# Kernel optimization log

Measured on AMD Instinct MI355X. Metric: run time of the kernel, lower is better.

Reference implementation:

```python
import jax, jax.numpy as jnp
import numpy as np

B, S, H, K = 8, 2048, 768, 128
FILTERS = (1, 3, 5)
C = H // len(FILTERS)  # 256 channels per conv, concat -> H
LN_EPS = 1e-05
COS_EPS = 1e-08


def setup_inputs() -> dict:
    key = jax.random.key(0)
    ks = jax.random.split(key, 16)
    mk = lambda k, shape: jax.random.normal(k, shape, dtype=jnp.float32) * 0.02
    return {
        "representation": jax.random.normal(ks[0], (B, S, H), dtype=jnp.float32),
        "src_mask": jnp.ones((B, S), dtype=jnp.float32),
        # conv weights stored as [k, H_in, C_out] for lax 1D conv (torch Conv2d(1,C,(k,H)))
        "enc_conv_w1": mk(ks[1], (1, H, C)),
        "enc_conv_w3": mk(ks[2], (3, H, C)),
        "enc_conv_w5": mk(ks[3], (5, H, C)),
        "ln_g": jnp.ones((H,), jnp.float32),
        "ln_b": jnp.zeros((H,), jnp.float32),
        "enc_lin_w": mk(ks[4], (H, H)),   # torch Linear weight [out,in]
        "enc_tr_w": mk(ks[5], (K, H)),
        "dec_tr_w": mk(ks[6], (H, K)),
        "dec_conv_w1": mk(ks[7], (1, H, C)),
        "dec_conv_w3": mk(ks[8], (3, H, C)),
        "dec_conv_w5": mk(ks[9], (5, H, C)),
        "dec_lin_w": mk(ks[10], (H, H)),
        "out_lin_w": mk(ks[11], (H, H)),
    }


def _multi_conv(x, ws):
    # x: [B, S, H]; each w: [k, H, C]; torch pads (k//2, 0) -> same-length for odd k
    outs = []
    for w in ws:
        k = w.shape[0]
        outs.append(jax.lax.conv_general_dilated(
            x, w, window_strides=(1,), padding=[(k // 2, k // 2)],
            dimension_numbers=("NWC", "WIO", "NWC")))
    return jnp.concatenate(outs, axis=-1)  # [B, S, H]


def _layernorm(x, g, b):
    mu = jnp.mean(x, axis=-1, keepdims=True)
    var = jnp.mean((x - mu) ** 2, axis=-1, keepdims=True)
    return (x - mu) * jax.lax.rsqrt(var + LN_EPS) * g + b


def reference(representation, src_mask, enc_conv_w1, enc_conv_w3, enc_conv_w5,
              ln_g, ln_b, enc_lin_w, enc_tr_w, dec_tr_w,
              dec_conv_w1, dec_conv_w3, dec_conv_w5, dec_lin_w, out_lin_w):
    # ---- AutoEncoder (dropout layers are identity in eval mode) ----
    h = _multi_conv(representation, (enc_conv_w1, enc_conv_w3, enc_conv_w5))
    h = _layernorm(h + representation, ln_g, ln_b)
    h = jnp.tanh(h @ enc_lin_w.T)
    location = h @ enc_tr_w.T            # [B, S, K] (encode_out)
    d = location @ dec_tr_w.T            # [B, S, H]
    d = _multi_conv(d, (dec_conv_w1, dec_conv_w3, dec_conv_w5))
    d = jnp.tanh(d @ dec_lin_w.T)
    decode_out = d @ out_lin_w.T         # [B, S, H]

    # ---- banded pairwise cosine similarity (fuses the torch shift loop) ----
    # torch loop writes dis_matrix[b, i, i+s+1] = cos(loc[b, i+s+1], loc[b, i])
    # for s in range(max_act_len), i.e. the strict upper band of the symmetric
    # pairwise cosine-similarity matrix with offsets 1..max_act_len.
    normed = location / jnp.maximum(
        jnp.sqrt(jnp.sum(location * location, axis=-1, keepdims=True)), COS_EPS)
    sim = jnp.einsum("bid,bjd->bij", normed, normed)  # [B, S, S]
    offs = jnp.arange(S)[None, :] - jnp.arange(S)[:, None]  # j - i
    max_act_len = jnp.max(jnp.sum(src_mask, axis=-1)).astype(jnp.int32)
    band = (offs >= 1) & (offs <= max_act_len)        # [S, S]
    dis_matrix = jnp.where(band[None], sim, 0.0)
    src_dis_mask = src_mask[:, :, None] * src_mask[:, None, :]
    act_dis_tags = band[None].astype(jnp.float32) * src_dis_mask
    return (location, dis_matrix, act_dis_tags, decode_out)
```

## Files before the change

### kernel.cpp

```cpp
#include <hip/hip_runtime.h>

#define B_   8
#define S_   2048
#define H_   768
#define K_   128
#define C_   256
#define SH_  2052
#define MTOK (B_*S_)

typedef __attribute__((ext_vector_type(8))) short short8;
typedef __attribute__((ext_vector_type(4))) float f32x4;

typedef __attribute__((address_space(1))) const void gvoid;
typedef __attribute__((address_space(3))) void lvoid;

__device__ __forceinline__ void gload16(const void* g, void* l) {
    __builtin_amdgcn_global_load_lds((gvoid*)g, (lvoid*)l, 16, 0, 0);
}

__device__ __forceinline__ ushort f2b(float f) {
    union { float f; unsigned u; } v; v.f = f;
    unsigned r = v.u + 0x7fffu + ((v.u >> 16) & 1u);
    return (ushort)(r >> 16);
}
__device__ __forceinline__ float b2f(ushort u) {
    union { unsigned u; float f; } v; v.u = ((unsigned)u) << 16;
    return v.f;
}
__device__ __forceinline__ float fast_tanh(float x) {
    float e = __expf(2.f * x);
    return 1.f - 2.f / (e + 1.f);
}


struct CvtE { const float* src; ushort* dst; int n; int kh; int sld; };

struct PrepP {
    const float* mask; int* Lp; ushort* lh;
    const float* rep;  ushort* xh;
    CvtE e[12];
};

__global__ __launch_bounds__(256) void k_prep(PrepP p) {
    const int tid = threadIdx.x;
    const int y = blockIdx.y;
    if (y == 0) {
        if (blockIdx.x == 0) {
            __shared__ float sh[4];
            float mx = 0.f;
            for (int b = 0; b < B_; ++b) {
                float s = 0.f;
                for (int q = tid; q < 512; q += 256) {
                    const float4 v = ((const float4*)(p.mask + b * S_))[q];
                    s += v.x + v.y + v.z + v.w;
                }
#pragma unroll
                for (int off = 32; off; off >>= 1) s += __shfl_xor(s, off);
                if ((tid & 63) == 0) sh[tid >> 6] = s;
                __syncthreads();
                if (tid == 0) mx = fmaxf(mx, sh[0] + sh[1] + sh[2] + sh[3]);
                __syncthreads();
            }
            if (tid == 0) *p.Lp = (int)mx;
            for (int i = tid; i < B_ * 4 * K_; i += 256) {
                const int b = i >> 9;
                const int rc = i & 511;
                const int rr = rc >> 7;
                const int cc = rc & 127;
                const int row = (rr < 2) ? rr : (2048 + rr);
                p.lh[((size_t)b * SH_ + row) * K_ + cc] = 0;
            }
        } else {
            int i = (blockIdx.x - 1) * 256 + tid;
            const int stride = (gridDim.x - 1) * 256;
            const int n4 = B_ * SH_ * H_ / 4;
            for (; i < n4; i += stride) {
                const int idx = i * 4;
                const int h = idx % H_;
                const int rs = idx / H_;
                const int s = rs % SH_;
                const int b = rs / SH_;
                ushort4 o; o.x = 0; o.y = 0; o.z = 0; o.w = 0;
                if (s >= 2 && s < S_ + 2) {
                    const float4 v = *(const float4*)(p.rep + ((size_t)b * S_ + (s - 2)) * H_ + h);
                    o.x = f2b(v.x); o.y = f2b(v.y); o.z = f2b(v.z); o.w = f2b(v.w);
                }
                *(ushort4*)(p.xh + idx) = o;
            }
        }
    } else {
        const CvtE e = p.e[y - 1];
        int i = blockIdx.x * 256 + tid;
        const int stride = gridDim.x * 256;
        for (; i < e.n; i += stride) {
            if (e.kh < 0) {
                e.dst[i] = 0;
            } else if (e.kh) {
                const int c = i / e.kh;
                const int r = i - c * e.kh;
                e.dst[i] = f2b(e.src[r * e.sld + c]);
            } else {
                e.dst[i] = f2b(e.src[i]);
            }
        }
    }
}


struct CompE { const ushort* w; int wld; int woff; ushort* o; int old_; int koff; };
struct CompP { const ushort* dtrT; CompE e[9]; };

__global__ __launch_bounds__(256) void k_compw(CompP p) {
    __shared__ __align__(16) ushort As[128 * 64];
    __shared__ __align__(16) ushort Bs[128 * 64];
    const CompE e = p.e[blockIdx.y];
    const int tid = threadIdx.x;
    const int w = tid >> 6, lane = tid & 63;
    const int l15 = lane & 15, lk = lane >> 4;
    const int wr = w >> 1, wc = w & 1;
    const int n_base = blockIdx.x * 128;
    f32x4 acc[4][4] = {};
    const int srow = lane >> 3;
    const int scol = (lane & 7) * 8;

    for (int kt = 0; kt < 12; ++kt) {
        const int kk = kt << 6;
#pragma unroll
        for (int q = 0; q < 4; ++q) {
            const int r = w * 32 + q * 8;
            gload16(p.dtrT + (size_t)(r + srow) * 768 + kk + scol, As + r * 64);
            gload16(e.w + (size_t)(n_base + r + srow) * e.wld + e.woff + kk + scol, Bs + r * 64);
        }
        __syncthreads();
#pragma unroll
        for (int ks = 0; ks < 2; ++ks) {
            short8 af[4], bfr[4];
#pragma unroll
            for (int i = 0; i < 4; ++i)
                af[i] = *(const short8*)(As + (wr * 64 + i * 16 + l15) * 64 + ks * 32 + 8 * lk);
#pragma unroll
            for (int j = 0; j < 4; ++j)
                bfr[j] = *(const short8*)(Bs + (wc * 64 + j * 16 + l15) * 64 + ks * 32 + 8 * lk);
#pragma unroll
            for (int i = 0; i < 4; ++i)
#pragma unroll
                for (int j = 0; j < 4; ++j)
                    acc[i][j] = __builtin_amdgcn_mfma_f32_16x16x32_bf16(af[i], bfr[j], acc[i][j], 0, 0, 0);
        }
        __syncthreads();
    }
#pragma unroll
    for (int i = 0; i < 4; ++i)
#pragma unroll
        for (int j = 0; j < 4; ++j)
#pragma unroll
            for (int jj = 0; jj < 4; ++jj) {
                const int jr = wr * 64 + i * 16 + 4 * lk + jj;
                const int c  = n_base + wc * 64 + j * 16 + l15;
                e.o[(size_t)c * e.old_ + e.koff + jr] = f2b(acc[i][j][jj]);
            }
}


struct G3P {
    const ushort* A;
    const ushort* W0;
    const ushort* W1;
    const ushort* W2;
    int lda;
    ushort* outB; int ldoB;
    int nMtiles;
};

__global__ __launch_bounds__(512, 2) void g3(G3P p) {
    constexpr int TPT = 12;
    constexpr int LDA = 768;
    constexpr int ASEG = 1024;
    constexpr int BSEG = 2048;
    constexpr int BUFE = (ASEG + BSEG) * 8;
    __shared__ __align__(16) ushort lds[3][BUFE];

    const int tid = threadIdx.x;
    const int w = tid >> 6, lane = tid & 63;
    const int l15 = lane & 15, lk = lane >> 4;
    const int wr = w >> 2, wc = w & 3;
    const int axor = l15 & 7;

    const int nM = p.nMtiles;
    int idx = blockIdx.x;
    int br;
    if (idx < nM) br = 2;
    else if (idx < 2 * nM) { br = 1; idx -= nM; }
    else { br = 0; idx -= 2 * nM; }
    idx = (idx & 7) * 16 + (idx >> 3);
    const int m_base = idx * 128;
    const int n_base = br * 256;
    const int nt = TPT * (2 * br + 1);
    const int Ktot = LDA * (2 * br + 1);
    const ushort* Wt = (br == 0) ? p.W0 : (br == 1) ? p.W1 : p.W2;
    const int arow0 = m_base + ((m_base >> 11) << 2) + (2 - br);

    auto stage1 = [&](int kt, int bufi, int q) {
        const int tap = kt / TPT;
        const int h0 = (kt - tap * TPT) << 6;
        if (q < 2) {
            const int seg = q * 512 + tid;
            const int row = seg >> 3;
            const int slot = (seg & 7) ^ (row & 7);
            gload16(p.A + (size_t)(arow0 + tap + row) * LDA + h0 + slot * 8,
                    &lds[bufi][seg * 8]);
        } else {
            const int seg = (q - 2) * 512 + tid;
            const int row = seg >> 3;
            const int slot = (seg & 7) ^ (row & 7);
            gload16(Wt + (size_t)row * Ktot + (kt << 6) + slot * 8,
                    &lds[bufi][ASEG * 8 + seg * 8]);
        }
    };
    auto stage = [&](int kt, int bufi) {
#pragma unroll
        for (int q = 0; q < 6; ++q) stage1(kt, bufi, q);
    };

    f32x4 acc[4][4] = {};

    stage(0, 0);
    stage(1, 1);

    int buf = 0;
    for (int t = 0; t < nt; ++t) {
        const ushort* Ab = &lds[buf][0];
        const ushort* Bb = &lds[buf][ASEG * 8];
        if (t + 1 < nt) asm volatile("s_waitcnt vmcnt(6)" ::: "memory");
        else            asm volatile("s_waitcnt vmcnt(0)" ::: "memory");
        __builtin_amdgcn_sched_barrier(0);
        asm volatile("s_barrier" ::: "memory");
        __builtin_amdgcn_sched_barrier(0);

        int nbuf = buf + 2; if (nbuf >= 3) nbuf -= 3;
        const bool sb = (t + 2 < nt);

#pragma unroll
        for (int ks = 0; ks < 2; ++ks) {
            short8 bq[4], aq[4];
#pragma unroll
            for (int ni = 0; ni < 4; ++ni)
                bq[ni] = *(const short8*)(Bb + (wc * 64 + ni * 16 + l15) * 64 + ((((ks << 2) | lk) ^ axor) << 3));
#pragma unroll
            for (int mi = 0; mi < 4; ++mi)
                aq[mi] = *(const short8*)(Ab + (wr * 64 + mi * 16 + l15) * 64 + ((((ks << 2) | lk) ^ axor) << 3));
            if (sb) { stage1(t + 2, nbuf, 3 * ks); stage1(t + 2, nbuf, 3 * ks + 1); stage1(t + 2, nbuf, 3 * ks + 2); }
            asm volatile("s_waitcnt lgkmcnt(0)" ::: "memory");
            __builtin_amdgcn_sched_barrier(0);
            __builtin_amdgcn_s_setprio(1);
#pragma unroll
            for (int mi = 0; mi < 4; ++mi)
#pragma unroll
                for (int ni = 0; ni < 4; ++ni)
                    acc[mi][ni] = __builtin_amdgcn_mfma_f32_16x16x32_bf16(aq[mi], bq[ni], acc[mi][ni], 0, 0, 0);
            __builtin_amdgcn_s_setprio(0);
            __builtin_amdgcn_sched_barrier(0);
        }
        ++buf; if (buf == 3) buf = 0;
    }

#pragma unroll
    for (int mi = 0; mi < 4; ++mi)
#pragma unroll
        for (int ni = 0; ni < 4; ++ni)
#pragma unroll
            for (int jj = 0; jj < 4; ++jj) {
                const int r = m_base + wr * 64 + mi * 16 + 4 * lk + jj;
                const int n = n_base + wc * 64 + ni * 16 + l15;
                p.outB[(size_t)r * p.ldoB + n] = f2b(acc[mi][ni][jj]);
            }
}


struct G4P {
    const ushort* A;
    const ushort* W;
    int Ktot;
    int lda;
    ushort* outB; int ldoB;
    float*  outF; int ldoF;
    int act;
    int haloA;
};

__global__ __launch_bounds__(256, 2) void g4(G4P p) {
    constexpr int ASEG = 1024;
    constexpr int BSEG = 1536;
    __shared__ __align__(16) ushort lds[2][(ASEG + BSEG) * 8];

    const int tid = threadIdx.x;
    const int w = tid >> 6, lane = tid & 63;
    const int l15 = lane & 15, lk = lane >> 4;
    const int wr = w >> 1, wc = w & 1;
    const int axor = l15 & 7;
    const int bx = (blockIdx.x & 7) * 16 + (blockIdx.x >> 3);
    const int m_base = bx * 128;
    const int n_base = blockIdx.y * 192;
    const int nt = p.Ktot >> 6;
    const int abase = p.haloA ? (m_base + ((m_base >> 11) << 2)) : m_base;

    auto stage = [&](int kt, int bufi) {
        const int kk = kt << 6;
        ushort* Ab = &lds[bufi][0];
        ushort* Bb = &lds[bufi][ASEG * 8];
#pragma unroll
        for (int q = 0; q < 4; ++q) {
            const int seg = q * 256 + tid;
            const int row = seg >> 3;
            const int s = (seg & 7) ^ (row & 7);
            gload16(p.A + (size_t)(abase + row) * p.lda + kk + s * 8, Ab + seg * 8);
        }
#pragma unroll
        for (int q = 0; q < 6; ++q) {
            const int seg = q * 256 + tid;
            const int row = seg >> 3;
            const int s = (seg & 7) ^ (row & 7);
            gload16(p.W + (size_t)(n_base + row) * p.Ktot + kk + s * 8, Bb + seg * 8);
        }
    };

    f32x4 acc[4][6] = {};

    stage(0, 0);
    stage(1, 1);

    for (int t = 0; t < nt; ++t) {
        const int cur = t & 1;
        const ushort* Ab = &lds[cur][0];
        const ushort* Bb = &lds[cur][ASEG * 8];
        if (t + 1 < nt) asm volatile("s_waitcnt vmcnt(10)" ::: "memory");
        else            asm volatile("s_waitcnt vmcnt(0)" ::: "memory");
        __builtin_amdgcn_sched_barrier(0);
        asm volatile("s_barrier" ::: "memory");
        __builtin_amdgcn_sched_barrier(0);

        short8 af[4][2], bf[6][2];
#pragma unroll
        for (int mi = 0; mi < 4; ++mi)
#pragma unroll
            for (int ks = 0; ks < 2; ++ks)
                af[mi][ks] = *(const short8*)(Ab + (wr * 64 + mi * 16 + l15) * 64 + ((((ks << 2) | lk) ^ axor) << 3));
#pragma unroll
        for (int ni = 0; ni < 6; ++ni)
#pragma unroll
            for (int ks = 0; ks < 2; ++ks)
                bf[ni][ks] = *(const short8*)(Bb + (wc * 96 + ni * 16 + l15) * 64 + ((((ks << 2) | lk) ^ axor) << 3));
        asm volatile("s_waitcnt lgkmcnt(0)" ::: "memory");
        __builtin_amdgcn_sched_barrier(0);
        asm volatile("s_barrier" ::: "memory");
        __builtin_amdgcn_sched_barrier(0);
        if (t + 2 < nt) stage(t + 2, cur);
        __builtin_amdgcn_sched_barrier(0);
        __builtin_amdgcn_s_setprio(1);
#pragma unroll
        for (int mi = 0; mi < 4; ++mi)
#pragma unroll
            for (int ni = 0; ni < 6; ++ni) {
                acc[mi][ni] = __builtin_amdgcn_mfma_f32_16x16x32_bf16(af[mi][0], bf[ni][0], acc[mi][ni], 0, 0, 0);
                acc[mi][ni] = __builtin_amdgcn_mfma_f32_16x16x32_bf16(af[mi][1], bf[ni][1], acc[mi][ni], 0, 0, 0);
            }
        __builtin_amdgcn_s_setprio(0);
        __builtin_amdgcn_sched_barrier(0);
    }

#pragma unroll
    for (int mi = 0; mi < 4; ++mi)
#pragma unroll
        for (int ni = 0; ni < 6; ++ni)
#pragma unroll
            for (int jj = 0; jj < 4; ++jj) {
                const int r = m_base + wr * 64 + mi * 16 + 4 * lk + jj;
                const int n = n_base + wc * 96 + ni * 16 + l15;
                float v = acc[mi][ni][jj];
                if (p.act) v = fast_tanh(v);
                if (p.outF) p.outF[(size_t)r * p.ldoF + n] = v;
                if (p.outB) p.outB[(size_t)r * p.ldoB + n] = f2b(v);
            }
}


struct GLP {
    const ushort* A;
    const ushort* Wt;
    float* outF;
    ushort* outH;
    ushort* outN;
};

__global__ __launch_bounds__(256) void gemm_loc(GLP p) {
    __shared__ __align__(16) ushort As[64 * 64];
    __shared__ __align__(16) ushort Bs[128 * 64];
    __shared__ float rowss[64][2];
    const int tid = threadIdx.x;
    const int w = tid >> 6, lane = tid & 63;
    const int l15 = lane & 15, lk = lane >> 4;
    const int bx = (blockIdx.x & 7) * 32 + (blockIdx.x >> 3);
    const int m_base = bx * 64;
    const int wr = w >> 1, wc = w & 1;
    f32x4 acc[2][4] = {};
    const int srow = lane >> 3;
    const int scol = (lane & 7) * 8;

    for (int kt = 0; kt < 12; ++kt) {
        const int kk = kt << 6;
#pragma unroll
        for (int q = 0; q < 2; ++q) {
            const int r = w * 16 + q * 8;
            gload16(p.A + (size_t)(m_base + r + srow) * H_ + kk + scol, As + r * 64);
        }
#pragma unroll
        for (int q = 0; q < 4; ++q) {
            const int r = w * 32 + q * 8;
            gload16(p.Wt + (size_t)(r + srow) * H_ + kk + scol, Bs + r * 64);
        }
        __syncthreads();
#pragma unroll
        for (int ks = 0; ks < 2; ++ks) {
            short8 af[2], bfr[4];
#pragma unroll
            for (int i = 0; i < 2; ++i)
                af[i] = *(const short8*)(As + (wr * 32 + i * 16 + l15) * 64 + ks * 32 + 8 * lk);
#pragma unroll
            for (int j = 0; j < 4; ++j)
                bfr[j] = *(const short8*)(Bs + (wc * 64 + j * 16 + l15) * 64 + ks * 32 + 8 * lk);
#pragma unroll
            for (int i = 0; i < 2; ++i)
#pragma unroll
                for (int j = 0; j < 4; ++j)
                    acc[i][j] = __builtin_amdgcn_mfma_f32_16x16x32_bf16(af[i], bfr[j], acc[i][j], 0, 0, 0);
        }
        __syncthreads();
    }

#pragma unroll
    for (int i = 0; i < 2; ++i)
#pragma unroll
        for (int jj = 0; jj < 4; ++jj) {
            float s = acc[i][0][jj] * acc[i][0][jj] + acc[i][1][jj] * acc[i][1][jj]
                    + acc[i][2][jj] * acc[i][2][jj] + acc[i][3][jj] * acc[i][3][jj];
#pragma unroll
            for (int off = 1; off < 16; off <<= 1) s += __shfl_xor(s, off);
            if (l15 == 0) rowss[wr * 32 + i * 16 + 4 * lk + jj][wc] = s;
        }
    __syncthreads();

    const int bb4 = ((m_base >> 11) << 2) + 2;
#pragma unroll
    for (int i = 0; i < 2; ++i)
#pragma unroll
        for (int j = 0; j < 4; ++j)
#pragma unroll
            for (int jj = 0; jj < 4; ++jj) {
                const int lr = wr * 32 + i * 16 + 4 * lk + jj;
                const int r  = m_base + lr;
                const int n  = wc * 64 + j * 16 + l15;
                const float v = acc[i][j][jj];
                const float ss = rowss[lr][0] + rowss[lr][1];
                const float sc = 1.f / fmaxf(sqrtf(ss), 1e-8f);
                p.outF[(size_t)r * K_ + n] = v;
                p.outH[(size_t)(r + bb4) * K_ + n] = f2b(v);
                p.outN[(size_t)r * K_ + n] = f2b(v * sc);
            }
}


__global__ __launch_bounds__(192) void k_ln(const ushort* __restrict__ conv,
                                            const float* __restrict__ rep,
                                            const float* __restrict__ gw,
                                            const float* __restrict__ bw,
                                            ushort* __restrict__ out) {
    const int row = blockIdx.x;
    const int tid = threadIdx.x;
    const int h = tid * 4;
    const ushort4 cv = *(const ushort4*)(conv + (size_t)row * H_ + h);
    const float4  rv = *(const float4*)(rep + (size_t)row * H_ + h);
    float v[4] = { b2f(cv.x) + rv.x, b2f(cv.y) + rv.y, b2f(cv.z) + rv.z, b2f(cv.w) + rv.w };
    float s1 = v[0] + v[1] + v[2] + v[3];
    float s2 = v[0]*v[0] + v[1]*v[1] + v[2]*v[2] + v[3]*v[3];
#pragma unroll
    for (int off = 32; off; off >>= 1) { s1 += __shfl_xor(s1, off); s2 += __shfl_xor(s2, off); }
    __shared__ float sh[6];
    const int wid = tid >> 6, lane = tid & 63;
    if (lane == 0) { sh[wid] = s1; sh[3 + wid] = s2; }
    __syncthreads();
    s1 = sh[0] + sh[1] + sh[2];
    s2 = sh[3] + sh[4] + sh[5];
    const float mu  = s1 * (1.f / H_);
    const float var = s2 * (1.f / H_) - mu * mu;
    const float rs  = rsqrtf(var + 1e-5f);
    const float4 gv = *(const float4*)(gw + h);
    const float4 bv = *(const float4*)(bw + h);
    ushort4 o;
    o.x = f2b((v[0] - mu) * rs * gv.x + bv.x);
    o.y = f2b((v[1] - mu) * rs * gv.y + bv.y);
    o.z = f2b((v[2] - mu) * rs * gv.z + bv.z);
    o.w = f2b((v[3] - mu) * rs * gv.w + bv.w);
    *(ushort4*)(out + (size_t)row * H_ + h) = o;
}


__global__ __launch_bounds__(256) void k_simtags(const ushort* __restrict__ normed,
                                                 const float* __restrict__ mask,
                                                 const int* __restrict__ Lp,
                                                 float* __restrict__ dis,
                                                 float* __restrict__ tags) {
    const int wid = threadIdx.x >> 6, lane = threadIdx.x & 63;
    const int l15 = lane & 15, lk = lane >> 4;
    const int b   = blockIdx.z;
    const int i0b = blockIdx.x * 64;
    const int i0  = i0b + wid * 16;
    const int j0  = blockIdx.y * 64;
    const int L   = *Lp;
    f32x4 acc[4] = {};
    if ((j0 + 63 >= i0b + 1) && (j0 <= i0b + 63 + L)) {
        const ushort* nb = normed + (size_t)b * S_ * K_;
#pragma unroll
        for (int kt = 0; kt < 4; ++kt) {
            const int kk = kt * 32;
            const short8 a = *(const short8*)(nb + (size_t)(i0 + l15) * K_ + kk + 8 * lk);
#pragma unroll
            for (int j = 0; j < 4; ++j) {
                const short8 bfr = *(const short8*)(nb + (size_t)(j0 + j * 16 + l15) * K_ + kk + 8 * lk);
                acc[j] = __builtin_amdgcn_mfma_f32_16x16x32_bf16(a, bfr, acc[j], 0, 0, 0);
            }
        }
    }
    const float* mb = mask + b * S_;
    float* dp = dis  + (size_t)b * S_ * S_;
    float* tp = tags + (size_t)b * S_ * S_;
#pragma unroll
    for (int j = 0; j < 4; ++j) {
#pragma unroll
        for (int jj = 0; jj < 4; ++jj) {
            const int i  = i0 + 4 * lk + jj;
            const int jc = j0 + j * 16 + l15;
            const int d  = jc - i;
            const bool band = (d >= 1 && d <= L);
            dp[(size_t)i * S_ + jc] = band ? acc[j][jj] : 0.f;
            tp[(size_t)i * S_ + jc] = band ? mb[i] * mb[jc] : 0.f;
        }
    }
}


extern "C" void kernel_launch(void* const* d_in, const int* in_sizes, int n_in,
                              void* d_out, int out_size, void* d_ws, size_t ws_size,
                              hipStream_t stream) {
    const float* rep  = (const float*)d_in[0];
    const float* mask = (const float*)d_in[1];
    const float* ew1  = (const float*)d_in[2];
    const float* ew3  = (const float*)d_in[3];
    const float* ew5  = (const float*)d_in[4];
    const float* lng  = (const float*)d_in[5];
    const float* lnb  = (const float*)d_in[6];
    const float* elin = (const float*)d_in[7];
    const float* etr  = (const float*)d_in[8];
    const float* dtr  = (const float*)d_in[9];
    const float* dw1  = (const float*)d_in[10];
    const float* dw3  = (const float*)d_in[11];
    const float* dw5  = (const float*)d_in[12];
    const float* dlin = (const float*)d_in[13];
    const float* olin = (const float*)d_in[14];

    float* out_loc = (float*)d_out;
    float* out_dis = out_loc + (size_t)B_ * S_ * K_;
    float* out_tag = out_dis + (size_t)B_ * S_ * S_;
    float* out_dec = out_tag + (size_t)B_ * S_ * S_;

    char* ws = (char*)d_ws;
    size_t off = 0;
    auto alloc = [&](size_t bytes) -> char* {
        char* p = ws + off;
        off += (bytes + 255) & ~(size_t)255;
        return p;
    };
    int*    Lp    = (int*)alloc(256);
    ushort* Xh    = (ushort*)alloc((size_t)B_ * SH_ * H_ * 2);
    ushort* bufLh = (ushort*)alloc((size_t)B_ * SH_ * K_ * 2);
    ushort* wte1  = (ushort*)alloc((size_t)C_ * 768 * 2);
    ushort* wte3  = (ushort*)alloc((size_t)C_ * 2304 * 2);
    ushort* wte5  = (ushort*)alloc((size_t)C_ * 3840 * 2);
    ushort* wtd1  = (ushort*)alloc((size_t)C_ * 768 * 2);
    ushort* wtd3  = (ushort*)alloc((size_t)C_ * 2304 * 2);
    ushort* wtd5  = (ushort*)alloc((size_t)C_ * 3840 * 2);
    ushort* welin = (ushort*)alloc((size_t)H_ * H_ * 2);
    ushort* wetr  = (ushort*)alloc((size_t)K_ * H_ * 2);
    ushort* dtrT  = (ushort*)alloc((size_t)K_ * H_ * 2);
    ushort* wdlin = (ushort*)alloc((size_t)H_ * H_ * 2);
    ushort* wolin = (ushort*)alloc((size_t)H_ * H_ * 2);
    ushort* Wc    = (ushort*)alloc((size_t)H_ * 640 * 2);
    ushort* bufB  = (ushort*)alloc((size_t)MTOK * H_ * 2);
    ushort* bufC  = (ushort*)alloc((size_t)MTOK * H_ * 2);
    ushort* bufD  = (ushort*)alloc((size_t)MTOK * H_ * 2);
    ushort* bufN  = (ushort*)alloc((size_t)MTOK * K_ * 2);
    if (ws_size < off) return;

    PrepP pp;
    pp.mask = mask; pp.Lp = Lp; pp.lh = bufLh;
    pp.rep = rep; pp.xh = Xh;
    pp.e[0]  = { ew1,  wte1, 768 * C_,  768,  C_ };
    pp.e[1]  = { ew3,  wte3, 2304 * C_, 2304, C_ };
    pp.e[2]  = { ew5,  wte5, 3840 * C_, 3840, C_ };
    pp.e[3]  = { dw1,  wtd1, 768 * C_,  768,  C_ };
    pp.e[4]  = { dw3,  wtd3, 2304 * C_, 2304, C_ };
    pp.e[5]  = { dw5,  wtd5, 3840 * C_, 3840, C_ };
    pp.e[6]  = { elin, welin, H_ * H_, 0, 0 };
    pp.e[7]  = { etr,  wetr,  K_ * H_, 0, 0 };
    pp.e[8]  = { dlin, wdlin, H_ * H_, 0, 0 };
    pp.e[9]  = { olin, wolin, H_ * H_, 0, 0 };
    pp.e[10] = { dtr,  dtrT,  K_ * H_, 768, K_ };
    pp.e[11] = { nullptr, Wc, H_ * 640, -1, 0 };
    k_prep<<<dim3(2048, 13), 256, 0, stream>>>(pp);

    {
        CompP cp; cp.dtrT = dtrT;
        cp.e[0] = { wtd1, 768,  0, Wc + (size_t)0 * 640,   640, 2 * 128 };
        for (int t = 0; t < 3; ++t)
            cp.e[1 + t] = { wtd3, 2304, t * 768, Wc + (size_t)256 * 640, 640, (1 + t) * 128 };
        for (int t = 0; t < 5; ++t)
            cp.e[4 + t] = { wtd5, 3840, t * 768, Wc + (size_t)512 * 640, 640, t * 128 };
        k_compw<<<dim3(2, 9), 256, 0, stream>>>(cp);
    }

    {
        G3P p{}; p.A = Xh; p.W0 = wte1; p.W1 = wte3; p.W2 = wte5;
        p.lda = H_; p.outB = bufB; p.ldoB = H_; p.nMtiles = MTOK / 128;
        g3<<<3 * (MTOK / 128), 512, 0, stream>>>(p);
    }
    k_ln<<<MTOK, 192, 0, stream>>>(bufB, rep, lng, lnb, bufC);
    {
        G4P p{}; p.A = bufC; p.W = welin; p.Ktot = H_; p.lda = H_;
        p.outB = bufD; p.ldoB = H_; p.act = 1;
        g4<<<dim3(MTOK / 128, H_ / 192), 256, 0, stream>>>(p);
    }
    {
        GLP p{ bufD, wetr, out_loc, bufLh, bufN };
        gemm_loc<<<MTOK / 64, 256, 0, stream>>>(p);
    }
    {
        G4P p{}; p.A = bufLh; p.W = Wc; p.Ktot = 640; p.lda = K_;
        p.outB = bufB; p.ldoB = H_; p.haloA = 1;
        g4<<<dim3(MTOK / 128, H_ / 192), 256, 0, stream>>>(p);
    }
    {
        G4P p{}; p.A = bufB; p.W = wdlin; p.Ktot = H_; p.lda = H_;
        p.outB = bufC; p.ldoB = H_; p.act = 1;
        g4<<<dim3(MTOK / 128, H_ / 192), 256, 0, stream>>>(p);
    }
    {
        G4P p{}; p.A = bufC; p.W = wolin; p.Ktot = H_; p.lda = H_;
        p.outF = out_dec; p.ldoF = H_;
        g4<<<dim3(MTOK / 128, H_ / 192), 256, 0, stream>>>(p);
    }
    k_simtags<<<dim3(S_ / 64, S_ / 64, B_), 256, 0, stream>>>(bufN, mask, Lp, out_dis, out_tag);
}
```

Before: 374.9 us.

## Shrink encoder conv GEMM tile to 64x256 with 256 threads and double buffering

Replaces the 512-thread 128x256-tile encoder conv kernel with a 256-thread 64x256-tile version that uses two LDS buffers instead of three. Each iteration now loads all fragments up front, synchronises, then issues the next stage's loads into the freed buffer before running the MFMAs. The change also drops the XCD-style block index swizzle in g4 and gemm_loc. Smaller tiles double the grid and may help occupancy and load balance across the three conv branches, but they lower weight reuse per tile and add an extra barrier per k-step.

```diff
diff --git a/kernel.cpp b/kernel.cpp
--- a/kernel.cpp
+++ b/kernel.cpp
@@ -169,57 +169,51 @@
     const ushort* W2;
     int lda;
     ushort* outB; int ldoB;
-    int nMtiles;
 };
 
-__global__ __launch_bounds__(512, 2) void g3(G3P p) {
+__global__ __launch_bounds__(256, 2) void g3b(G3P p) {
     constexpr int TPT = 12;
     constexpr int LDA = 768;
-    constexpr int ASEG = 1024;
+    constexpr int ASEG = 512;
     constexpr int BSEG = 2048;
-    constexpr int BUFE = (ASEG + BSEG) * 8;
-    __shared__ __align__(16) ushort lds[3][BUFE];
+    __shared__ __align__(16) ushort lds[2][(ASEG + BSEG) * 8];
 
     const int tid = threadIdx.x;
-    const int w = tid >> 6, lane = tid & 63;
+    const int wc = tid >> 6, lane = tid & 63;
     const int l15 = lane & 15, lk = lane >> 4;
-    const int wr = w >> 2, wc = w & 3;
     const int axor = l15 & 7;
 
-    const int nM = p.nMtiles;
     int idx = blockIdx.x;
     int br;
-    if (idx < nM) br = 2;
-    else if (idx < 2 * nM) { br = 1; idx -= nM; }
-    else { br = 0; idx -= 2 * nM; }
-    idx = (idx & 7) * 16 + (idx >> 3);
-    const int m_base = idx * 128;
+    if (idx < 256) br = 2;
+    else if (idx < 512) { br = 1; idx -= 256; }
+    else { br = 0; idx -= 512; }
+    const int m_base = idx * 64;
     const int n_base = br * 256;
     const int nt = TPT * (2 * br + 1);
     const int Ktot = LDA * (2 * br + 1);
     const ushort* Wt = (br == 0) ? p.W0 : (br == 1) ? p.W1 : p.W2;
     const int arow0 = m_base + ((m_base >> 11) << 2) + (2 - br);
 
-    auto stage1 = [&](int kt, int bufi, int q) {
+    auto stage = [&](int kt, int bufi) {
         const int tap = kt / TPT;
         const int h0 = (kt - tap * TPT) << 6;
-        if (q < 2) {
-            const int seg = q * 512 + tid;
+        ushort* Ab = &lds[bufi][0];
+        ushort* Bb = &lds[bufi][ASEG * 8];
+#pragma unroll
+        for (int q = 0; q < 2; ++q) {
+            const int seg = q * 256 + tid;
             const int row = seg >> 3;
-            const int slot = (seg & 7) ^ (row & 7);
-            gload16(p.A + (size_t)(arow0 + tap + row) * LDA + h0 + slot * 8,
-                    &lds[bufi][seg * 8]);
-        } else {
-            const int seg = (q - 2) * 512 + tid;
+            const int s = (seg & 7) ^ (row & 7);
+            gload16(p.A + (size_t)(arow0 + tap + row) * LDA + h0 + s * 8, Ab + seg * 8);
+        }
+#pragma unroll
+        for (int q = 0; q < 8; ++q) {
+            const int seg = q * 256 + tid;
             const int row = seg >> 3;
-            const int slot = (seg & 7) ^ (row & 7);
-            gload16(Wt + (size_t)row * Ktot + (kt << 6) + slot * 8,
-                    &lds[bufi][ASEG * 8 + seg * 8]);
-        }
-    };
-    auto stage = [&](int kt, int bufi) {
-#pragma unroll
-        for (int q = 0; q < 6; ++q) stage1(kt, bufi, q);
+            const int s = (seg & 7) ^ (row & 7);
+            gload16(Wt + (size_t)row * Ktot + (kt << 6) + s * 8, Bb + seg * 8);
+        }
     };
 
     f32x4 acc[4][4] = {};
@@ -227,41 +221,43 @@
     stage(0, 0);
     stage(1, 1);
 
-    int buf = 0;
     for (int t = 0; t < nt; ++t) {
-        const ushort* Ab = &lds[buf][0];
-        const ushort* Bb = &lds[buf][ASEG * 8];
-        if (t + 1 < nt) asm volatile("s_waitcnt vmcnt(6)" ::: "memory");
+        const int cur = t & 1;
+        const ushort* Ab = &lds[cur][0];
+        const ushort* Bb = &lds[cur][ASEG * 8];
+        if (t + 1 < nt) asm volatile("s_waitcnt vmcnt(10)" ::: "memory");
         else            asm volatile("s_waitcnt vmcnt(0)" ::: "memory");
         __builtin_amdgcn_sched_barrier(0);
         asm volatile("s_barrier" ::: "memory");
         __builtin_amdgcn_sched_barrier(0);
 
-        int nbuf = buf + 2; if (nbuf >= 3) nbuf -= 3;
-        const bool sb = (t + 2 < nt);
-
-#pragma unroll
-        for (int ks = 0; ks < 2; ++ks) {
-            short8 bq[4], aq[4];
-#pragma unroll
-            for (int ni = 0; ni < 4; ++ni)
-                bq[ni] = *(const short8*)(Bb + (wc * 64 + ni * 16 + l15) * 64 + ((((ks << 2) | lk) ^ axor) << 3));
-#pragma unroll
-            for (int mi = 0; mi < 4; ++mi)
-                aq[mi] = *(const short8*)(Ab + (wr * 64 + mi * 16 + l15) * 64 + ((((ks << 2) | lk) ^ axor) << 3));
-            if (sb) { stage1(t + 2, nbuf, 3 * ks); stage1(t + 2, nbuf, 3 * ks + 1); stage1(t + 2, nbuf, 3 * ks + 2); }
-            asm volatile("s_waitcnt lgkmcnt(0)" ::: "memory");
-            __builtin_amdgcn_sched_barrier(0);
-            __builtin_amdgcn_s_setprio(1);
-#pragma unroll
-            for (int mi = 0; mi < 4; ++mi)
-#pragma unroll
-                for (int ni = 0; ni < 4; ++ni)
-                    acc[mi][ni] = __builtin_amdgcn_mfma_f32_16x16x32_bf16(aq[mi], bq[ni], acc[mi][ni], 0, 0, 0);
-            __builtin_amdgcn_s_setprio(0);
-            __builtin_amdgcn_sched_barrier(0);
-        }
-        ++buf; if (buf == 3) buf = 0;
+        short8 af[4][2], bf[4][2];
+#pragma unroll
+        for (int mi = 0; mi < 4; ++mi)
+#pragma unroll
+            for (int ks = 0; ks < 2; ++ks)
+                af[mi][ks] = *(const short8*)(Ab + (mi * 16 + l15) * 64 + ((((ks << 2) | lk) ^ axor) << 3));
+#pragma unroll
+        for (int ni = 0; ni < 4; ++ni)
+#pragma unroll
+            for (int ks = 0; ks < 2; ++ks)
+                bf[ni][ks] = *(const short8*)(Bb + (wc * 64 + ni * 16 + l15) * 64 + ((((ks << 2) | lk) ^ axor) << 3));
+        asm volatile("s_waitcnt lgkmcnt(0)" ::: "memory");
+        __builtin_amdgcn_sched_barrier(0);
+        asm volatile("s_barrier" ::: "memory");
+        __builtin_amdgcn_sched_barrier(0);
+        if (t + 2 < nt) stage(t + 2, cur);
+        __builtin_amdgcn_sched_barrier(0);
+        __builtin_amdgcn_s_setprio(1);
+#pragma unroll
+        for (int mi = 0; mi < 4; ++mi)
+#pragma unroll
+            for (int ni = 0; ni < 4; ++ni) {
+                acc[mi][ni] = __builtin_amdgcn_mfma_f32_16x16x32_bf16(af[mi][0], bf[ni][0], acc[mi][ni], 0, 0, 0);
+                acc[mi][ni] = __builtin_amdgcn_mfma_f32_16x16x32_bf16(af[mi][1], bf[ni][1], acc[mi][ni], 0, 0, 0);
+            }
+        __builtin_amdgcn_s_setprio(0);
+        __builtin_amdgcn_sched_barrier(0);
     }
 
 #pragma unroll
@@ -270,7 +266,7 @@
         for (int ni = 0; ni < 4; ++ni)
 #pragma unroll
             for (int jj = 0; jj < 4; ++jj) {
-                const int r = m_base + wr * 64 + mi * 16 + 4 * lk + jj;
+                const int r = m_base + mi * 16 + 4 * lk + jj;
                 const int n = n_base + wc * 64 + ni * 16 + l15;
                 p.outB[(size_t)r * p.ldoB + n] = f2b(acc[mi][ni][jj]);
             }
@@ -298,8 +294,7 @@
     const int l15 = lane & 15, lk = lane >> 4;
     const int wr = w >> 1, wc = w & 1;
     const int axor = l15 & 7;
-    const int bx = (blockIdx.x & 7) * 16 + (blockIdx.x >> 3);
-    const int m_base = bx * 128;
+    const int m_base = blockIdx.x * 128;
     const int n_base = blockIdx.y * 192;
     const int nt = p.Ktot >> 6;
     const int abase = p.haloA ? (m_base + ((m_base >> 11) << 2)) : m_base;
@@ -399,8 +394,7 @@
     const int tid = threadIdx.x;
     const int w = tid >> 6, lane = tid & 63;
     const int l15 = lane & 15, lk = lane >> 4;
-    const int bx = (blockIdx.x & 7) * 32 + (blockIdx.x >> 3);
-    const int m_base = bx * 64;
+    const int m_base = blockIdx.x * 64;
     const int wr = w >> 1, wc = w & 1;
     f32x4 acc[2][4] = {};
     const int srow = lane >> 3;
@@ -629,8 +623,8 @@
 
     {
         G3P p{}; p.A = Xh; p.W0 = wte1; p.W1 = wte3; p.W2 = wte5;
-        p.lda = H_; p.outB = bufB; p.ldoB = H_; p.nMtiles = MTOK / 128;
-        g3<<<3 * (MTOK / 128), 512, 0, stream>>>(p);
+        p.lda = H_; p.outB = bufB; p.ldoB = H_;
+        g3b<<<768, 256, 0, stream>>>(p);
     }
     k_ln<<<MTOK, 192, 0, stream>>>(bufB, rep, lng, lnb, bufC);
     {
```

After: 383.6 us. 1.02x slower.

## Fold decoder linear weight into composed conv weight, removing one GEMM

Applied to the files above, without the earlier changes.

Precomputes Wz = dec_lin_w × (composed decoder transform+conv weight) with a new small GEMM kernel. The decoder conv GEMM and the following dec_lin GEMM become one K=640 GEMM with tanh applied directly. This removes a full 16K×768×768 GEMM and one intermediate buffer round-trip. It also drops the block-index swizzles in g3, g4 and gemm_loc, which changes L2 locality, and adds an extra bf16 rounding of the combined weight.

```diff
diff --git a/kernel.cpp b/kernel.cpp
--- a/kernel.cpp
+++ b/kernel.cpp
@@ -157,7 +157,61 @@
             for (int jj = 0; jj < 4; ++jj) {
                 const int jr = wr * 64 + i * 16 + 4 * lk + jj;
                 const int c  = n_base + wc * 64 + j * 16 + l15;
-                e.o[(size_t)c * e.old_ + e.koff + jr] = f2b(acc[i][j][jj]);
+                e.o[(size_t)(e.koff + jr) * e.old_ + c] = f2b(acc[i][j][jj]);
+            }
+}
+
+
+__global__ __launch_bounds__(256) void k_wz(const ushort* __restrict__ wdlin,
+                                            const ushort* __restrict__ WcT,
+                                            ushort* __restrict__ Wz) {
+    __shared__ __align__(16) ushort As[128 * 64];
+    __shared__ __align__(16) ushort Bs[128 * 64];
+    const int tid = threadIdx.x;
+    const int w = tid >> 6, lane = tid & 63;
+    const int l15 = lane & 15, lk = lane >> 4;
+    const int wr = w >> 1, wc = w & 1;
+    const int m_base = blockIdx.x * 128;
+    const int n_base = blockIdx.y * 128;
+    f32x4 acc[4][4] = {};
+    const int srow = lane >> 3;
+    const int scol = (lane & 7) * 8;
+
+    for (int kt = 0; kt < 12; ++kt) {
+        const int kk = kt << 6;
+#pragma unroll
+        for (int q = 0; q < 4; ++q) {
+            const int r = w * 32 + q * 8;
+            gload16(wdlin + (size_t)(m_base + r + srow) * 768 + kk + scol, As + r * 64);
+            gload16(WcT + (size_t)(n_base + r + srow) * 768 + kk + scol, Bs + r * 64);
+        }
+        __syncthreads();
+#pragma unroll
+        for (int ks = 0; ks < 2; ++ks) {
+            short8 af[4], bfr[4];
+#pragma unroll
+            for (int i = 0; i < 4; ++i)
+                af[i] = *(const short8*)(As + (wr * 64 + i * 16 + l15) * 64 + ks * 32 + 8 * lk);
+#pragma unroll
+            for (int j = 0; j < 4; ++j)
+                bfr[j] = *(const short8*)(Bs + (wc * 64 + j * 16 + l15) * 64 + ks * 32 + 8 * lk);
+#pragma unroll
+            for (int i = 0; i < 4; ++i)
+#pragma unroll
+                for (int j = 0; j < 4; ++j)
+                    acc[i][j] = __builtin_amdgcn_mfma_f32_16x16x32_bf16(af[i], bfr[j], acc[i][j], 0, 0, 0);
+        }
+        __syncthreads();
+    }
+#pragma unroll
+    for (int i = 0; i < 4; ++i)
+#pragma unroll
+        for (int j = 0; j < 4; ++j)
+#pragma unroll
+            for (int jj = 0; jj < 4; ++jj) {
+                const int o = m_base + wr * 64 + i * 16 + 4 * lk + jj;
+                const int k = n_base + wc * 64 + j * 16 + l15;
+                Wz[(size_t)o * 640 + k] = f2b(acc[i][j][jj]);
             }
 }
 
@@ -192,7 +246,6 @@
     if (idx < nM) br = 2;
     else if (idx < 2 * nM) { br = 1; idx -= nM; }
     else { br = 0; idx -= 2 * nM; }
-    idx = (idx & 7) * 16 + (idx >> 3);
     const int m_base = idx * 128;
     const int n_base = br * 256;
     const int nt = TPT * (2 * br + 1);
@@ -298,8 +351,7 @@
     const int l15 = lane & 15, lk = lane >> 4;
     const int wr = w >> 1, wc = w & 1;
     const int axor = l15 & 7;
-    const int bx = (blockIdx.x & 7) * 16 + (blockIdx.x >> 3);
-    const int m_base = bx * 128;
+    const int m_base = blockIdx.x * 128;
     const int n_base = blockIdx.y * 192;
     const int nt = p.Ktot >> 6;
     const int abase = p.haloA ? (m_base + ((m_base >> 11) << 2)) : m_base;
@@ -399,8 +451,7 @@
     const int tid = threadIdx.x;
     const int w = tid >> 6, lane = tid & 63;
     const int l15 = lane & 15, lk = lane >> 4;
-    const int bx = (blockIdx.x & 7) * 32 + (blockIdx.x >> 3);
-    const int m_base = bx * 64;
+    const int m_base = blockIdx.x * 64;
     const int wr = w >> 1, wc = w & 1;
     f32x4 acc[2][4] = {};
     const int srow = lane >> 3;
@@ -593,7 +644,8 @@
     ushort* dtrT  = (ushort*)alloc((size_t)K_ * H_ * 2);
     ushort* wdlin = (ushort*)alloc((size_t)H_ * H_ * 2);
     ushort* wolin = (ushort*)alloc((size_t)H_ * H_ * 2);
-    ushort* Wc    = (ushort*)alloc((size_t)H_ * 640 * 2);
+    ushort* WcT   = (ushort*)alloc((size_t)640 * H_ * 2);
+    ushort* Wz    = (ushort*)alloc((size_t)H_ * 640 * 2);
     ushort* bufB  = (ushort*)alloc((size_t)MTOK * H_ * 2);
     ushort* bufC  = (ushort*)alloc((size_t)MTOK * H_ * 2);
     ushort* bufD  = (ushort*)alloc((size_t)MTOK * H_ * 2);
@@ -614,18 +666,19 @@
     pp.e[8]  = { dlin, wdlin, H_ * H_, 0, 0 };
     pp.e[9]  = { olin, wolin, H_ * H_, 0, 0 };
     pp.e[10] = { dtr,  dtrT,  K_ * H_, 768, K_ };
-    pp.e[11] = { nullptr, Wc, H_ * 640, -1, 0 };
+    pp.e[11] = { nullptr, WcT, 640 * H_, -1, 0 };
     k_prep<<<dim3(2048, 13), 256, 0, stream>>>(pp);
 
     {
         CompP cp; cp.dtrT = dtrT;
-        cp.e[0] = { wtd1, 768,  0, Wc + (size_t)0 * 640,   640, 2 * 128 };
+        cp.e[0] = { wtd1, 768,  0, WcT + 0,   768, 2 * 128 };
         for (int t = 0; t < 3; ++t)
-            cp.e[1 + t] = { wtd3, 2304, t * 768, Wc + (size_t)256 * 640, 640, (1 + t) * 128 };
+            cp.e[1 + t] = { wtd3, 2304, t * 768, WcT + 256, 768, (1 + t) * 128 };
         for (int t = 0; t < 5; ++t)
-            cp.e[4 + t] = { wtd5, 3840, t * 768, Wc + (size_t)512 * 640, 640, t * 128 };
+            cp.e[4 + t] = { wtd5, 3840, t * 768, WcT + 512, 768, t * 128 };
         k_compw<<<dim3(2, 9), 256, 0, stream>>>(cp);
     }
+    k_wz<<<dim3(H_ / 128, 640 / 128), 256, 0, stream>>>(wdlin, WcT, Wz);
 
     {
         G3P p{}; p.A = Xh; p.W0 = wte1; p.W1 = wte3; p.W2 = wte5;
@@ -643,13 +696,8 @@
         gemm_loc<<<MTOK / 64, 256, 0, stream>>>(p);
     }
     {
-        G4P p{}; p.A = bufLh; p.W = Wc; p.Ktot = 640; p.lda = K_;
-        p.outB = bufB; p.ldoB = H_; p.haloA = 1;
-        g4<<<dim3(MTOK / 128, H_ / 192), 256, 0, stream>>>(p);
-    }
-    {
-        G4P p{}; p.A = bufB; p.W = wdlin; p.Ktot = H_; p.lda = H_;
-        p.outB = bufC; p.ldoB = H_; p.act = 1;
+        G4P p{}; p.A = bufLh; p.W = Wz; p.Ktot = 640; p.lda = K_;
+        p.outB = bufC; p.ldoB = H_; p.act = 1; p.haloA = 1;
         g4<<<dim3(MTOK / 128, H_ / 192), 256, 0, stream>>>(p);
     }
     {
```

New measurement: 370.1 us (median of 2 runs). About the same (-1.3%).
